# Optimization experiments

Hardware: AMD Instinct MI355X
Metric: run time of the kernel (lower is better)

Reference implementation:

```python
import jax, jax.numpy as jnp
import numpy as np

H, NH, L, S, B, V = 512, 8, 6, 2048, 2, 32000
DH = H // NH
EPS = 1e-5


def posenc(h, s):
    pos = jnp.arange(s, dtype=jnp.float32)[:, None]
    div = jnp.power(10000.0, jnp.arange(0, h, 2, dtype=jnp.float32) / h)
    pe = jnp.zeros((s, h), dtype=jnp.float32)
    pe = pe.at[:, 0::2].set(jnp.sin(pos / div))
    pe = pe.at[:, 1::2].set(jnp.cos(pos / div))
    return pe


def layernorm(x, g, b):
    mu = jnp.mean(x, axis=-1, keepdims=True)
    var = jnp.mean(jnp.square(x - mu), axis=-1, keepdims=True)
    return (x - mu) * jax.lax.rsqrt(var + EPS) * g + b


def setup_inputs() -> dict:
    key = jax.random.key(0)
    ks = jax.random.split(key, 16)
    sc = 0.02
    return {
        "src": jax.random.randint(ks[0], (B, S), 0, V),
        "mask": jnp.ones((B, 1, 1, S), dtype=jnp.int32),
        "emb": jax.random.normal(ks[1], (V, H), jnp.float32) * sc,
        "Wq": jax.random.normal(ks[2], (L, H, H), jnp.float32) * sc,
        "bq": jnp.zeros((L, H), jnp.float32),
        "Wk": jax.random.normal(ks[3], (L, H, H), jnp.float32) * sc,
        "bk": jnp.zeros((L, H), jnp.float32),
        "Wv": jax.random.normal(ks[4], (L, H, H), jnp.float32) * sc,
        "bv": jnp.zeros((L, H), jnp.float32),
        "Wo": jax.random.normal(ks[5], (L, H, H), jnp.float32) * sc,
        "bo": jnp.zeros((L, H), jnp.float32),
        "gamma": jnp.ones((L, H), jnp.float32),
        "beta": jnp.zeros((L, H), jnp.float32),
        "W1": jax.random.normal(ks[6], (L, H, 4 * H), jnp.float32) * sc,
        "b1": jnp.zeros((L, 4 * H), jnp.float32),
        "W2": jax.random.normal(ks[7], (L, 4 * H, H), jnp.float32) * sc,
        "b2": jnp.zeros((L, H), jnp.float32),
    }


def reference(src, mask, emb, Wq, bq, Wk, bk, Wv, bv, Wo, bo, gamma, beta, W1, b1, W2, b2):
    x = emb[src] + posenc(H, S)[None, :, :]  # [B,S,H]
    for i in range(L):
        q = (x @ Wq[i] + bq[i]).reshape(B, S, NH, DH).transpose(0, 2, 1, 3)
        k = (x @ Wk[i] + bk[i]).reshape(B, S, NH, DH).transpose(0, 2, 1, 3)
        v = (x @ Wv[i] + bv[i]).reshape(B, S, NH, DH).transpose(0, 2, 1, 3)
        scores = jnp.einsum("bhqd,bhkd->bhqk", q, k) / jnp.sqrt(jnp.float32(DH))
        scores = jnp.where(mask == 0, jnp.float32(-1e20), scores)
        attn = jax.nn.softmax(scores, axis=-1)
        av = jnp.einsum("bhqk,bhkd->bhqd", attn, v)
        attn_out = av.transpose(0, 2, 1, 3).reshape(B, S, H) @ Wo[i] + bo[i]
        # NOTE: same LayerNorm params applied to both sublayers (as in source)
        res = x + layernorm(attn_out, gamma[i], beta[i])
        ffn = jax.nn.relu(res @ W1[i] + b1[i]) @ W2[i] + b2[i]
        x = res + layernorm(ffn, gamma[i], beta[i])
    return x
```

## Files before the change

kernel.cpp:

```cpp
#include <hip/hip_runtime.h>
#include <math.h>

#define HDIM 512
#define NHEAD 8
#define NLAYER 6
#define SEQ 2048
#define BATCH 2
#define DHEAD 64
#define TOKENS (BATCH*SEQ)
#define FFND (4*HDIM)
#define QSTR 1536

typedef unsigned short u16;
typedef unsigned long long u64;
typedef __attribute__((ext_vector_type(8))) short short8;
typedef __attribute__((ext_vector_type(4))) float f32x4;

__device__ __forceinline__ u16 f2b(float f) {
  unsigned u = __float_as_uint(f);
  u += 0x7FFFu + ((u >> 16) & 1u);
  return (u16)(u >> 16);
}

__device__ __forceinline__ unsigned cvtpk_bf16(float lo, float hi) {
  unsigned r;
  asm("v_cvt_pk_bf16_f32 %0, %1, %2" : "=v"(r) : "v"(lo), "v"(hi));
  return r;
}

__device__ __forceinline__ void gload_lds16(const u16* g, u16* l) {
  __builtin_amdgcn_global_load_lds((const __attribute__((address_space(1))) void*)g,
                                   (__attribute__((address_space(3))) void*)l, 16, 0, 0);
}

__global__ void embed_pe(const int* __restrict__ src, const float* __restrict__ emb,
                         float* __restrict__ X, u16* __restrict__ Xb) {
  int tok = blockIdx.x;
  int lane = threadIdx.x;
  int s = tok & (SEQ - 1);
  int c0 = lane * 8;
  const float* e = emb + (long)src[tok] * HDIM + c0;
  float v[8];
#pragma unroll
  for (int j = 0; j < 8; j++) {
    int c = c0 + j;
    float arg = (float)s * exp2f(-(float)(c & ~1) * 0.02595256917f);
    v[j] = e[j] + ((c & 1) ? cosf(arg) : sinf(arg));
  }
  float* xp = X + (long)tok * HDIM + c0;
#pragma unroll
  for (int j = 0; j < 8; j++) xp[j] = v[j];
  u16 hb[8];
#pragma unroll
  for (int j = 0; j < 8; j++) hb[j] = f2b(v[j]);
  uint4 pk;
  pk.x = hb[0] | ((unsigned)hb[1] << 16);
  pk.y = hb[2] | ((unsigned)hb[3] << 16);
  pk.z = hb[4] | ((unsigned)hb[5] << 16);
  pk.w = hb[6] | ((unsigned)hb[7] << 16);
  *(uint4*)(Xb + (long)tok * HDIM + c0) = pk;
}

__global__ void maskprep(const int* __restrict__ mask, u64* __restrict__ mb) {
  int t = threadIdx.x;
  int b = t >> 5, tile = t & 31;
  const int* m = mask + b * SEQ + tile * 64;
  u64 w = 0;
#pragma unroll
  for (int j = 0; j < 64; j++) w |= (u64)(m[j] != 0) << j;
  mb[t] = w;
}

__global__ __launch_bounds__(256) void prep_weights(
    const float* __restrict__ Wq, const float* __restrict__ Wk, const float* __restrict__ Wv,
    const float* __restrict__ Wo, const float* __restrict__ W1, const float* __restrict__ W2,
    const float* __restrict__ bq, const float* __restrict__ bk, const float* __restrict__ bv,
    u16* __restrict__ Wqkvt, u16* __restrict__ Wot, u16* __restrict__ W1t, u16* __restrict__ W2t,
    float* __restrict__ bqkv) {
  int t = blockIdx.x;
  int tid = threadIdx.x;
  if (t == 768) {
    for (int i = tid; i < 1536; i += 256)
      bqkv[i] = (i < 512) ? bq[i] : (i < 1024) ? bk[i - 512] : bv[i - 1024];
    return;
  }
  const float* src; u16* dst; int K, N, kt, nt; long drow0 = 0;
  if (t < 192)      { int m = t / 64, r = t % 64; src = (m==0)?Wq:(m==1)?Wk:Wv; dst = Wqkvt; drow0 = (long)m*512; K=512;  N=512;  kt=r/8;  nt=r%8; }
  else if (t < 256) { int r = t - 192; src = Wo; dst = Wot; K=512;  N=512;  kt=r/8;  nt=r%8; }
  else if (t < 512) { int r = t - 256; src = W1; dst = W1t; K=512;  N=2048; kt=r/32; nt=r%32; }
  else              { int r = t - 512; src = W2; dst = W2t; K=2048; N=512;  kt=r/8;  nt=r%8; }
  __shared__ __align__(16) u16 Lt[64 * 72];
  int kl = tid >> 2;
#pragma unroll
  for (int rr = 0; rr < 4; rr++) {
    int cl = (tid & 3) * 4 + rr * 16;
    float4 v = *(const float4*)(src + (long)(kt * 64 + kl) * N + nt * 64 + cl);
    Lt[(cl + 0) * 72 + kl] = f2b(v.x);
    Lt[(cl + 1) * 72 + kl] = f2b(v.y);
    Lt[(cl + 2) * 72 + kl] = f2b(v.z);
    Lt[(cl + 3) * 72 + kl] = f2b(v.w);
  }
  __syncthreads();
  int nl = tid >> 2;
  int kc = (tid & 3) * 16;
  u16* dp = dst + (drow0 + nt * 64 + nl) * (long)K + kt * 64 + kc;
  *(uint4*)dp       = *(const uint4*)&Lt[nl * 72 + kc];
  *(uint4*)(dp + 8) = *(const uint4*)&Lt[nl * 72 + kc + 8];
}

__global__ __launch_bounds__(256) void vtranspose(const u16* __restrict__ QKV,
                                                  u16* __restrict__ Vtb) {
  __shared__ __align__(16) u16 Lt[64 * 72];
  int tid = threadIdx.x;
  int bh = blockIdx.y, b = bh >> 3, h = bh & 7;
  int s0 = blockIdx.x * 64;
  const u16* vsrc = QKV + (long)(b * SEQ + s0) * QSTR + 1024 + h * DHEAD;
  int key = tid >> 2, dc = (tid & 3) * 16;
  const u16* vp = vsrc + (long)key * QSTR + dc;
  uint4 v0 = *(const uint4*)vp;
  uint4 v1 = *(const uint4*)(vp + 8);
  unsigned vr[8] = { v0.x, v0.y, v0.z, v0.w, v1.x, v1.y, v1.z, v1.w };
#pragma unroll
  for (int j = 0; j < 8; j++) {
    Lt[(dc + 2 * j) * 72 + key]     = (u16)vr[j];
    Lt[(dc + 2 * j + 1) * 72 + key] = (u16)(vr[j] >> 16);
  }
  __syncthreads();
  int d = tid >> 2, kc = (tid & 3) * 16;
  u16* dst = Vtb + ((long)bh * DHEAD + d) * SEQ + s0 + kc;
  *(uint4*)dst       = *(const uint4*)&Lt[d * 72 + kc];
  *(uint4*)(dst + 8) = *(const uint4*)&Lt[d * 72 + kc + 8];
}

template <int BM, int BN, bool RELU, bool WF32, bool WB16>
__global__ __launch_bounds__(256) void gemm_tn(const u16* __restrict__ A,
                                               const u16* __restrict__ Bt,
                                               const float* __restrict__ bias,
                                               float* __restrict__ Cf,
                                               u16* __restrict__ Cb,
                                               int M, int N, int K) {
  constexpr int NF = BN / 32;
  constexpr int MF = BM / 32;
  __shared__ __align__(16) u16 As[2][BM * 32];
  __shared__ __align__(16) u16 Bs[2][BN * 32];
  int tid = threadIdx.x;
  int wave = tid >> 6, lane = tid & 63;
  int ln = lane & 15, hi = lane >> 4;
  int wm = wave >> 1, wn = wave & 1;
  int m0 = blockIdx.y * BM, n0 = blockIdx.x * BN;

  f32x4 acc[MF][NF] = {};

  int srow = lane >> 2;
  int skc  = (lane & 3) * 8;

  auto issue = [&](int kt, int buf) {
    int k0 = kt * 32;
#pragma unroll
    for (int j = 0; j < BM / 64; j++) {
      int row = (wave * (BM / 64) + j) * 16 + srow;
      gload_lds16(A + (long)(m0 + row) * K + k0 + skc, &As[buf][row * 32 + skc]);
    }
#pragma unroll
    for (int j = 0; j < BN / 64; j++) {
      int row = (wave * (BN / 64) + j) * 16 + srow;
      gload_lds16(Bt + (long)(n0 + row) * K + k0 + skc, &Bs[buf][row * 32 + skc]);
    }
  };

  int NT = K / 32;
  issue(0, 0);
  __syncthreads();
  for (int kt = 0; kt < NT; kt++) {
    int buf = kt & 1;
    if (kt + 1 < NT) issue(kt + 1, buf ^ 1);
    short8 af[MF], bf[NF];
#pragma unroll
    for (int mt = 0; mt < MF; mt++)
      af[mt] = *(const short8*)&As[buf][(wm * (BM / 2) + mt * 16 + ln) * 32 + 8 * hi];
#pragma unroll
    for (int nt = 0; nt < NF; nt++)
      bf[nt] = *(const short8*)&Bs[buf][(wn * (BN / 2) + nt * 16 + ln) * 32 + 8 * hi];
#pragma unroll
    for (int mt = 0; mt < MF; mt++)
#pragma unroll
      for (int nt = 0; nt < NF; nt++)
        acc[mt][nt] = __builtin_amdgcn_mfma_f32_16x16x32_bf16(af[mt], bf[nt], acc[mt][nt], 0, 0, 0);
    __syncthreads();
  }

#pragma unroll
  for (int mt = 0; mt < MF; mt++)
#pragma unroll
    for (int nt = 0; nt < NF; nt++)
#pragma unroll
      for (int r = 0; r < 4; r++) {
        int row = m0 + wm * (BM / 2) + mt * 16 + hi * 4 + r;
        int col = n0 + wn * (BN / 2) + nt * 16 + ln;
        float v = acc[mt][nt][r] + bias[col];
        if (RELU) v = fmaxf(v, 0.0f);
        if (WF32) Cf[(long)row * N + col] = v;
        if (WB16) Cb[(long)row * N + col] = f2b(v);
      }
}

__global__ __launch_bounds__(256) void attention(const u16* __restrict__ QKV,
                                                 const u16* __restrict__ Vtb,
                                                 const u64* __restrict__ maskb,
                                                 float* __restrict__ Opart,
                                                 float* __restrict__ Lpart) {
  __shared__ __align__(16) u16 Ks[2][64 * 64];
  __shared__ __align__(16) u16 Vs[2][64 * 64];
  __shared__ u64 Msk[SEQ / 64];
  int tid = threadIdx.x, w = tid >> 6, lane = tid & 63;
  int ln = lane & 15, hi = lane >> 4;
  int h0 = hi & 1, h1 = hi >> 1, ln7 = ln & 7;
  int lin = blockIdx.x;
  int lid = (lin & 7) * 128 + (lin >> 3);
  int bh = lid >> 6, qt = (lid >> 1) & 31, kz = lid & 1;
  int b = bh >> 3, h = bh & 7;
  int q0 = qt * 64 + w * 16;
  const u16* qbase = QKV + (long)b * SEQ * QSTR + h * DHEAD;
  const u16* kbase = qbase + 512;
  const u16* vtbase = Vtb + (long)bh * DHEAD * SEQ;

  short8 qf[2];
#pragma unroll
  for (int ks = 0; ks < 2; ks++)
    qf[ks] = *(const short8*)(qbase + (long)(q0 + ln) * QSTR + ks * 32 + 8 * hi);

  u64 mw0 = 0;
  if (tid < SEQ / 64) mw0 = maskb[b * (SEQ / 64) + tid];

  int sr0 = tid >> 3, sc = tid & 7;
  const u16 *kp0, *kp1, *vp0, *vp1;
  {
    int r1 = sr0 + 32;
    int key0 = (sr0 & 7) | ((sr0 & 0x18) << 1) | ((sr0 & 0x20) >> 2);
    int key1 = (r1 & 7) | ((r1 & 0x18) << 1) | ((r1 & 0x20) >> 2);
    kp0 = kbase + (long)key0 * QSTR + (sc ^ (sr0 & 7)) * 8;
    kp1 = kbase + (long)key1 * QSTR + (sc ^ (r1 & 7)) * 8;
    vp0 = vtbase + (long)sr0 * SEQ + (sc ^ (sr0 & 7)) * 8;
    vp1 = vtbase + (long)r1 * SEQ + (sc ^ (r1 & 7)) * 8;
  }
  int d0 = sr0 * 64 + sc * 8, d1 = d0 + 2048;

  auto issue = [&](int t, int buf) {
    long ko = (long)t * (64 * QSTR);
    int vo = t * 64;
    gload_lds16(kp0 + ko, &Ks[buf][d0]);
    gload_lds16(kp1 + ko, &Ks[buf][d1]);
    gload_lds16(vp0 + vo, &Vs[buf][d0]);
    gload_lds16(vp1 + vo, &Vs[buf][d1]);
  };

  f32x4 o[4] = {};
  float lsum = 0.0f;
  const int t0 = kz * 16;
  const int NTL = 16;

  issue(t0, 0);
  issue(t0 + 1, 1);
  if (tid < SEQ / 64) Msk[tid] = mw0;
  asm volatile("s_waitcnt vmcnt(4)" ::: "memory");
  __builtin_amdgcn_sched_barrier(0);
  __builtin_amdgcn_s_barrier();
  __builtin_amdgcn_sched_barrier(0);

  for (int ti = 0; ti < NTL; ti++) {
    int buf = ti & 1;
    u64 mw = Msk[t0 + ti];

    f32x4 s[4] = {};
    __builtin_amdgcn_s_setprio(1);
#pragma unroll
    for (int ks = 0; ks < 2; ks++)
#pragma unroll
      for (int kb = 0; kb < 4; kb++) {
        short8 kf = *(const short8*)&Ks[buf][(kb * 16 + ln) * 64 + (((ks << 2) + hi) ^ ln7) * 8];
        s[kb] = __builtin_amdgcn_mfma_f32_16x16x32_bf16(kf, qf[ks], s[kb], 0, 0, 0);
      }
    __builtin_amdgcn_s_setprio(0);

    unsigned D[4][2];
    if (mw == 0xFFFFFFFFFFFFFFFFull) {
#pragma unroll
      for (int kb = 0; kb < 4; kb++) {
        float p[4];
#pragma unroll
        for (int r = 0; r < 4; r++) {
          float pv = __expf(s[kb][r] * 0.125f);
          lsum += pv;
          p[r] = pv;
        }
        D[kb][0] = cvtpk_bf16(p[0], p[1]);
        D[kb][1] = cvtpk_bf16(p[2], p[3]);
      }
    } else {
      unsigned shb = h1 * 16 + h0 * 4;
      u64 mws = mw >> shb;
      unsigned nib[4] = { (unsigned)mws & 0xFu, (unsigned)(mws >> 32) & 0xFu,
                          (unsigned)(mws >> 8) & 0xFu, (unsigned)(mws >> 40) & 0xFu };
#pragma unroll
      for (int kb = 0; kb < 4; kb++) {
        float p[4];
#pragma unroll
        for (int r = 0; r < 4; r++) {
          float pv = __expf(s[kb][r] * 0.125f);
          pv = ((nib[kb] >> r) & 1u) ? pv : 0.0f;
          lsum += pv;
          p[r] = pv;
        }
        D[kb][0] = cvtpk_bf16(p[0], p[1]);
        D[kb][1] = cvtpk_bf16(p[2], p[3]);
      }
    }

    short8 pb[2];
#pragma unroll
    for (int ks = 0; ks < 2; ks++) {
      unsigned own0 = h0 ? D[2 + ks][0] : D[ks][0];
      unsigned own1 = h0 ? D[2 + ks][1] : D[ks][1];
      unsigned snd0 = h0 ? D[ks][0] : D[2 + ks][0];
      unsigned snd1 = h0 ? D[ks][1] : D[2 + ks][1];
      unsigned rc0 = (unsigned)__shfl_xor((int)snd0, 16);
      unsigned rc1 = (unsigned)__shfl_xor((int)snd1, 16);
      union { unsigned u[4]; short8 v; } pu;
      pu.u[0] = h0 ? rc0 : own0;
      pu.u[1] = h0 ? rc1 : own1;
      pu.u[2] = h0 ? own0 : rc0;
      pu.u[3] = h0 ? own1 : rc1;
      pb[ks] = pu.v;
    }

    __builtin_amdgcn_s_setprio(1);
#pragma unroll
    for (int ks = 0; ks < 2; ks++)
#pragma unroll
      for (int mb = 0; mb < 4; mb++) {
        short8 vf = *(const short8*)&Vs[buf][(mb * 16 + ln) * 64 + (((ks << 2) + hi) ^ ln7) * 8];
        o[mb] = __builtin_amdgcn_mfma_f32_16x16x32_bf16(vf, pb[ks], o[mb], 0, 0, 0);
      }
    __builtin_amdgcn_s_setprio(0);

    asm volatile("s_waitcnt lgkmcnt(0)" ::: "memory");
    __builtin_amdgcn_sched_barrier(0);
    __builtin_amdgcn_s_barrier();
    __builtin_amdgcn_sched_barrier(0);
    if (ti + 2 < NTL) {
      issue(t0 + ti + 2, buf);
      asm volatile("s_waitcnt vmcnt(4)" ::: "memory");
    } else {
      asm volatile("s_waitcnt vmcnt(0)" ::: "memory");
    }
    __builtin_amdgcn_sched_barrier(0);
    __builtin_amdgcn_s_barrier();
    __builtin_amdgcn_sched_barrier(0);
  }

  lsum += __shfl_xor(lsum, 16);
  lsum += __shfl_xor(lsum, 32);

  float* OpB = Opart + (long)lid * 4096 + w * 1024;
#pragma unroll
  for (int mb = 0; mb < 4; mb++)
    *(f32x4*)&OpB[ln * 64 + mb * 16 + hi * 4] = o[mb];
  if (hi == 0) Lpart[(long)lid * 64 + w * 16 + ln] = lsum;
}

__global__ __launch_bounds__(256) void attn_merge(const float* __restrict__ Op,
                                                  const float* __restrict__ Lp,
                                                  u16* __restrict__ Og) {
  int lin = blockIdx.x;
  int mlid = (lin & 7) * 64 + (lin >> 3);
  int bh = mlid >> 5, qt = mlid & 31;
  int b = bh >> 3, h = bh & 7;
  int tid = threadIdx.x;
  __shared__ float Ls[64];
  if (tid < 64) Ls[tid] = 1.0f / (Lp[(long)mlid * 128 + tid] + Lp[(long)mlid * 128 + 64 + tid]);
  __syncthreads();
  const float* P0 = Op + (long)mlid * 8192;
  const float* P1 = P0 + 4096;
  u16* obase = Og + (long)b * SEQ * HDIM + (long)qt * 64 * HDIM + h * DHEAD;
#pragma unroll
  for (int j = 0; j < 4; j++) {
    int flat = j * 1024 + tid * 4;
    int row = flat >> 6, c = flat & 63;
    float4 a = *(const float4*)&P0[flat];
    float4 bb = *(const float4*)&P1[flat];
    float rl = Ls[row];
    uint2 val;
    val.x = cvtpk_bf16((a.x + bb.x) * rl, (a.y + bb.y) * rl);
    val.y = cvtpk_bf16((a.z + bb.z) * rl, (a.w + bb.w) * rl);
    *(uint2*)(obase + (long)row * HDIM + c) = val;
  }
}

__global__ __launch_bounds__(256) void ln_residual(const float* __restrict__ Xin,
                                                   const float* __restrict__ T0,
                                                   const float* __restrict__ gamma,
                                                   const float* __restrict__ beta,
                                                   float* __restrict__ Xout,
                                                   u16* __restrict__ Xb) {
  int tid = threadIdx.x, w = tid >> 6, lane = tid & 63;
  int row = blockIdx.x * 4 + w;
  const float* t0 = T0 + (long)row * HDIM;
  int c0 = lane * 8;
  float v[8];
  {
    float4 a0 = *(const float4*)(t0 + c0);
    float4 b0 = *(const float4*)(t0 + c0 + 4);
    v[0] = a0.x; v[1] = a0.y; v[2] = a0.z; v[3] = a0.w;
    v[4] = b0.x; v[5] = b0.y; v[6] = b0.z; v[7] = b0.w;
  }
  float sum = 0.0f;
#pragma unroll
  for (int j = 0; j < 8; j++) sum += v[j];
#pragma unroll
  for (int off = 32; off; off >>= 1) sum += __shfl_xor(sum, off);
  float mu = sum * (1.0f / HDIM);
  float sq = 0.0f;
#pragma unroll
  for (int j = 0; j < 8; j++) { float d = v[j] - mu; sq += d * d; }
#pragma unroll
  for (int off = 32; off; off >>= 1) sq += __shfl_xor(sq, off);
  float rs = rsqrtf(sq * (1.0f / HDIM) + 1e-5f);
  const float* xin = Xin + (long)row * HDIM + c0;
  float* xout = Xout + (long)row * HDIM + c0;
  u16 hb[8];
#pragma unroll
  for (int j = 0; j < 8; j++) {
    int c = c0 + j;
    float y = xin[j] + (v[j] - mu) * rs * gamma[c] + beta[c];
    xout[j] = y;
    hb[j] = f2b(y);
  }
  uint4 pk;
  pk.x = hb[0] | ((unsigned)hb[1] << 16);
  pk.y = hb[2] | ((unsigned)hb[3] << 16);
  pk.z = hb[4] | ((unsigned)hb[5] << 16);
  pk.w = hb[6] | ((unsigned)hb[7] << 16);
  *(uint4*)(Xb + (long)row * HDIM + c0) = pk;
}

extern "C" void kernel_launch(void* const* d_in, const int* in_sizes, int n_in,
                              void* d_out, int out_size, void* d_ws, size_t ws_size,
                              hipStream_t stream) {
  const int*   src   = (const int*)d_in[0];
  const int*   mask  = (const int*)d_in[1];
  const float* emb   = (const float*)d_in[2];
  const float* Wq    = (const float*)d_in[3];
  const float* bq    = (const float*)d_in[4];
  const float* Wk    = (const float*)d_in[5];
  const float* bk    = (const float*)d_in[6];
  const float* Wv    = (const float*)d_in[7];
  const float* bv    = (const float*)d_in[8];
  const float* Wo    = (const float*)d_in[9];
  const float* bo    = (const float*)d_in[10];
  const float* gamma = (const float*)d_in[11];
  const float* beta  = (const float*)d_in[12];
  const float* W1    = (const float*)d_in[13];
  const float* b1    = (const float*)d_in[14];
  const float* W2    = (const float*)d_in[15];
  const float* b2    = (const float*)d_in[16];

  char* ws = (char*)d_ws;
  float* X     = (float*)(ws);
  u16*   Xb    = (u16*)(ws + (8ll << 20));
  u16*   QKVb  = (u16*)(ws + (12ll << 20));
  u16*   Mb    = (u16*)(ws + (12ll << 20));
  u16*   AVb   = (u16*)(ws + (24ll << 20));
  float* T     = (float*)(ws + (28ll << 20));
  u16*   Wqkvt = (u16*)(ws + (44ll << 20));
  u16*   Wot   = (u16*)(ws + (45ll << 20) + (512ll << 10));
  u16*   W1t   = (u16*)(ws + (46ll << 20));
  u16*   W2t   = (u16*)(ws + (48ll << 20));
  float* bqkv  = (float*)(ws + (50ll << 20));
  float* Lpart = (float*)(ws + (50ll << 20) + (512ll << 10));
  u16*   Vtb   = (u16*)(ws + (51ll << 20));
  u64*   maskbits = (u64*)(ws + (55ll << 20));
  float* Opart = T;

  embed_pe<<<dim3(TOKENS), dim3(64), 0, stream>>>(src, emb, X, Xb);
  maskprep<<<dim3(1), dim3(64), 0, stream>>>(mask, maskbits);

  for (int i = 0; i < NLAYER; i++) {
    long wo = (long)i * HDIM * HDIM;
    prep_weights<<<dim3(769), 256, 0, stream>>>(
        Wq + wo, Wk + wo, Wv + wo, Wo + wo,
        W1 + (long)i * HDIM * FFND, W2 + (long)i * FFND * HDIM,
        bq + i * HDIM, bk + i * HDIM, bv + i * HDIM,
        Wqkvt, Wot, W1t, W2t, bqkv);

    gemm_tn<128, 128, false, false, true><<<dim3(QSTR / 128, TOKENS / 128), 256, 0, stream>>>(
        Xb, Wqkvt, bqkv, nullptr, QKVb, TOKENS, QSTR, HDIM);

    vtranspose<<<dim3(SEQ / 64, BATCH * NHEAD), 256, 0, stream>>>(QKVb, Vtb);

    attention<<<dim3(1024), 256, 0, stream>>>(QKVb, Vtb, maskbits, Opart, Lpart);

    attn_merge<<<dim3(512), 256, 0, stream>>>(Opart, Lpart, AVb);

    gemm_tn<64, 64, false, true, false><<<dim3(HDIM / 64, TOKENS / 64), 256, 0, stream>>>(
        AVb, Wot, bo + i * HDIM, T, nullptr, TOKENS, HDIM, HDIM);

    ln_residual<<<dim3(TOKENS / 4), 256, 0, stream>>>(X, T, gamma + i * HDIM,
                                                      beta + i * HDIM, X, Xb);

    gemm_tn<128, 128, true, false, true><<<dim3(FFND / 128, TOKENS / 128), 256, 0, stream>>>(
        Xb, W1t, b1 + (long)i * FFND, nullptr, Mb, TOKENS, FFND, HDIM);

    gemm_tn<64, 64, false, true, false><<<dim3(HDIM / 64, TOKENS / 64), 256, 0, stream>>>(
        Mb, W2t, b2 + i * HDIM, T, nullptr, TOKENS, HDIM, FFND);

    ln_residual<<<dim3(TOKENS / 4), 256, 0, stream>>>(X, T, gamma + i * HDIM,
                                                      beta + i * HDIM, X, Xb);
  }

  hipMemcpyAsync(d_out, X, (size_t)TOKENS * HDIM * sizeof(float),
                 hipMemcpyDeviceToDevice, stream);
}
```

Measured before the change: 946.1 us.

## Double query rows per warp and split attention keys four ways

Each attention block now covers 128 query rows (32 per warp, as two 16-row groups) instead of 64, and the key sequence is split into four chunks of 8 tiles instead of two chunks of 16. Every K/V fragment loaded from LDS now feeds two MFMAs, which halves LDS traffic per FLOP and adds independent MFMA chains. The trade-off is more registers per thread and twice the partial-output traffic, since the merge kernel now sums four partials. Opart moves to its own workspace region because it has grown to twice its former size.

```diff
diff --git a/kernel.cpp b/kernel.cpp
--- a/kernel.cpp
+++ b/kernel.cpp
@@ -217,17 +217,20 @@
   int h0 = hi & 1, h1 = hi >> 1, ln7 = ln & 7;
   int lin = blockIdx.x;
   int lid = (lin & 7) * 128 + (lin >> 3);
-  int bh = lid >> 6, qt = (lid >> 1) & 31, kz = lid & 1;
+  int bh = lid >> 6, rem = lid & 63;
+  int qt = rem >> 2, kz = rem & 3;
   int b = bh >> 3, h = bh & 7;
-  int q0 = qt * 64 + w * 16;
+  int q0 = qt * 128 + w * 32;
   const u16* qbase = QKV + (long)b * SEQ * QSTR + h * DHEAD;
   const u16* kbase = qbase + 512;
   const u16* vtbase = Vtb + (long)bh * DHEAD * SEQ;
 
-  short8 qf[2];
-#pragma unroll
-  for (int ks = 0; ks < 2; ks++)
-    qf[ks] = *(const short8*)(qbase + (long)(q0 + ln) * QSTR + ks * 32 + 8 * hi);
+  short8 qf[2][2];
+#pragma unroll
+  for (int qg = 0; qg < 2; qg++)
+#pragma unroll
+    for (int ks = 0; ks < 2; ks++)
+      qf[qg][ks] = *(const short8*)(qbase + (long)(q0 + qg * 16 + ln) * QSTR + ks * 32 + 8 * hi);
 
   u64 mw0 = 0;
   if (tid < SEQ / 64) mw0 = maskb[b * (SEQ / 64) + tid];
@@ -254,10 +257,10 @@
     gload_lds16(vp1 + vo, &Vs[buf][d1]);
   };
 
-  f32x4 o[4] = {};
-  float lsum = 0.0f;
-  const int t0 = kz * 16;
-  const int NTL = 16;
+  f32x4 o[2][4] = {};
+  float lsum[2] = {0.0f, 0.0f};
+  const int t0 = kz * 8;
+  const int NTL = 8;
 
   issue(t0, 0);
   issue(t0 + 1, 1);
@@ -271,76 +274,82 @@
     int buf = ti & 1;
     u64 mw = Msk[t0 + ti];
 
-    f32x4 s[4] = {};
+    f32x4 s[2][4] = {};
     __builtin_amdgcn_s_setprio(1);
 #pragma unroll
     for (int ks = 0; ks < 2; ks++)
 #pragma unroll
       for (int kb = 0; kb < 4; kb++) {
         short8 kf = *(const short8*)&Ks[buf][(kb * 16 + ln) * 64 + (((ks << 2) + hi) ^ ln7) * 8];
-        s[kb] = __builtin_amdgcn_mfma_f32_16x16x32_bf16(kf, qf[ks], s[kb], 0, 0, 0);
+        s[0][kb] = __builtin_amdgcn_mfma_f32_16x16x32_bf16(kf, qf[0][ks], s[0][kb], 0, 0, 0);
+        s[1][kb] = __builtin_amdgcn_mfma_f32_16x16x32_bf16(kf, qf[1][ks], s[1][kb], 0, 0, 0);
       }
     __builtin_amdgcn_s_setprio(0);
 
-    unsigned D[4][2];
+    unsigned D[2][4][2];
     if (mw == 0xFFFFFFFFFFFFFFFFull) {
 #pragma unroll
-      for (int kb = 0; kb < 4; kb++) {
-        float p[4];
-#pragma unroll
-        for (int r = 0; r < 4; r++) {
-          float pv = __expf(s[kb][r] * 0.125f);
-          lsum += pv;
-          p[r] = pv;
+      for (int qg = 0; qg < 2; qg++)
+#pragma unroll
+        for (int kb = 0; kb < 4; kb++) {
+          float p[4];
+#pragma unroll
+          for (int r = 0; r < 4; r++) {
+            float pv = __expf(s[qg][kb][r] * 0.125f);
+            lsum[qg] += pv;
+            p[r] = pv;
+          }
+          D[qg][kb][0] = cvtpk_bf16(p[0], p[1]);
+          D[qg][kb][1] = cvtpk_bf16(p[2], p[3]);
         }
-        D[kb][0] = cvtpk_bf16(p[0], p[1]);
-        D[kb][1] = cvtpk_bf16(p[2], p[3]);
-      }
     } else {
       unsigned shb = h1 * 16 + h0 * 4;
       u64 mws = mw >> shb;
       unsigned nib[4] = { (unsigned)mws & 0xFu, (unsigned)(mws >> 32) & 0xFu,
                           (unsigned)(mws >> 8) & 0xFu, (unsigned)(mws >> 40) & 0xFu };
 #pragma unroll
-      for (int kb = 0; kb < 4; kb++) {
-        float p[4];
-#pragma unroll
-        for (int r = 0; r < 4; r++) {
-          float pv = __expf(s[kb][r] * 0.125f);
-          pv = ((nib[kb] >> r) & 1u) ? pv : 0.0f;
-          lsum += pv;
-          p[r] = pv;
+      for (int qg = 0; qg < 2; qg++)
+#pragma unroll
+        for (int kb = 0; kb < 4; kb++) {
+          float p[4];
+#pragma unroll
+          for (int r = 0; r < 4; r++) {
+            float pv = __expf(s[qg][kb][r] * 0.125f);
+            pv = ((nib[kb] >> r) & 1u) ? pv : 0.0f;
+            lsum[qg] += pv;
+            p[r] = pv;
+          }
+          D[qg][kb][0] = cvtpk_bf16(p[0], p[1]);
+          D[qg][kb][1] = cvtpk_bf16(p[2], p[3]);
         }
-        D[kb][0] = cvtpk_bf16(p[0], p[1]);
-        D[kb][1] = cvtpk_bf16(p[2], p[3]);
+    }
+
+    __builtin_amdgcn_s_setprio(1);
+#pragma unroll
+    for (int ks = 0; ks < 2; ks++) {
+      short8 pb[2];
+#pragma unroll
+      for (int qg = 0; qg < 2; qg++) {
+        unsigned own0 = h0 ? D[qg][2 + ks][0] : D[qg][ks][0];
+        unsigned own1 = h0 ? D[qg][2 + ks][1] : D[qg][ks][1];
+        unsigned snd0 = h0 ? D[qg][ks][0] : D[qg][2 + ks][0];
+        unsigned snd1 = h0 ? D[qg][ks][1] : D[qg][2 + ks][1];
+        unsigned rc0 = (unsigned)__shfl_xor((int)snd0, 16);
+        unsigned rc1 = (unsigned)__shfl_xor((int)snd1, 16);
+        union { unsigned u[4]; short8 v; } pu;
+        pu.u[0] = h0 ? rc0 : own0;
+        pu.u[1] = h0 ? rc1 : own1;
+        pu.u[2] = h0 ? own0 : rc0;
+        pu.u[3] = h0 ? own1 : rc1;
+        pb[qg] = pu.v;
+      }
+#pragma unroll
+      for (int mb = 0; mb < 4; mb++) {
+        short8 vf = *(const short8*)&Vs[buf][(mb * 16 + ln) * 64 + (((ks << 2) + hi) ^ ln7) * 8];
+        o[0][mb] = __builtin_amdgcn_mfma_f32_16x16x32_bf16(vf, pb[0], o[0][mb], 0, 0, 0);
+        o[1][mb] = __builtin_amdgcn_mfma_f32_16x16x32_bf16(vf, pb[1], o[1][mb], 0, 0, 0);
       }
     }
-
-    short8 pb[2];
-#pragma unroll
-    for (int ks = 0; ks < 2; ks++) {
-      unsigned own0 = h0 ? D[2 + ks][0] : D[ks][0];
-      unsigned own1 = h0 ? D[2 + ks][1] : D[ks][1];
-      unsigned snd0 = h0 ? D[ks][0] : D[2 + ks][0];
-      unsigned snd1 = h0 ? D[ks][1] : D[2 + ks][1];
-      unsigned rc0 = (unsigned)__shfl_xor((int)snd0, 16);
-      unsigned rc1 = (unsigned)__shfl_xor((int)snd1, 16);
-      union { unsigned u[4]; short8 v; } pu;
-      pu.u[0] = h0 ? rc0 : own0;
-      pu.u[1] = h0 ? rc1 : own1;
-      pu.u[2] = h0 ? own0 : rc0;
-      pu.u[3] = h0 ? own1 : rc1;
-      pb[ks] = pu.v;
-    }
-
-    __builtin_amdgcn_s_setprio(1);
-#pragma unroll
-    for (int ks = 0; ks < 2; ks++)
-#pragma unroll
-      for (int mb = 0; mb < 4; mb++) {
-        short8 vf = *(const short8*)&Vs[buf][(mb * 16 + ln) * 64 + (((ks << 2) + hi) ^ ln7) * 8];
-        o[mb] = __builtin_amdgcn_mfma_f32_16x16x32_bf16(vf, pb[ks], o[mb], 0, 0, 0);
-      }
     __builtin_amdgcn_s_setprio(0);
 
     asm volatile("s_waitcnt lgkmcnt(0)" ::: "memory");
@@ -358,40 +367,54 @@
     __builtin_amdgcn_sched_barrier(0);
   }
 
-  lsum += __shfl_xor(lsum, 16);
-  lsum += __shfl_xor(lsum, 32);
-
-  float* OpB = Opart + (long)lid * 4096 + w * 1024;
-#pragma unroll
-  for (int mb = 0; mb < 4; mb++)
-    *(f32x4*)&OpB[ln * 64 + mb * 16 + hi * 4] = o[mb];
-  if (hi == 0) Lpart[(long)lid * 64 + w * 16 + ln] = lsum;
+#pragma unroll
+  for (int qg = 0; qg < 2; qg++) {
+    lsum[qg] += __shfl_xor(lsum[qg], 16);
+    lsum[qg] += __shfl_xor(lsum[qg], 32);
+  }
+
+  float* OpB = Opart + (long)lid * 8192 + w * 2048;
+#pragma unroll
+  for (int qg = 0; qg < 2; qg++)
+#pragma unroll
+    for (int mb = 0; mb < 4; mb++)
+      *(f32x4*)&OpB[(qg * 16 + ln) * 64 + mb * 16 + hi * 4] = o[qg][mb];
+  if (hi == 0) {
+    Lpart[(long)lid * 128 + w * 32 + ln]      = lsum[0];
+    Lpart[(long)lid * 128 + w * 32 + 16 + ln] = lsum[1];
+  }
 }
 
 __global__ __launch_bounds__(256) void attn_merge(const float* __restrict__ Op,
                                                   const float* __restrict__ Lp,
                                                   u16* __restrict__ Og) {
   int lin = blockIdx.x;
-  int mlid = (lin & 7) * 64 + (lin >> 3);
-  int bh = mlid >> 5, qt = mlid & 31;
+  int mlid = (lin & 7) * 32 + (lin >> 3);
+  int bh = mlid >> 4, qt = mlid & 15;
   int b = bh >> 3, h = bh & 7;
   int tid = threadIdx.x;
-  __shared__ float Ls[64];
-  if (tid < 64) Ls[tid] = 1.0f / (Lp[(long)mlid * 128 + tid] + Lp[(long)mlid * 128 + 64 + tid]);
+  __shared__ float Ls[128];
+  long lbase = (long)mlid * 4 * 128;
+  if (tid < 128) {
+    float l = Lp[lbase + tid] + Lp[lbase + 128 + tid] +
+              Lp[lbase + 256 + tid] + Lp[lbase + 384 + tid];
+    Ls[tid] = 1.0f / l;
+  }
   __syncthreads();
-  const float* P0 = Op + (long)mlid * 8192;
-  const float* P1 = P0 + 4096;
-  u16* obase = Og + (long)b * SEQ * HDIM + (long)qt * 64 * HDIM + h * DHEAD;
-#pragma unroll
-  for (int j = 0; j < 4; j++) {
+  const float* P0 = Op + (long)mlid * 4 * 8192;
+  u16* obase = Og + (long)b * SEQ * HDIM + (long)qt * 128 * HDIM + h * DHEAD;
+#pragma unroll
+  for (int j = 0; j < 8; j++) {
     int flat = j * 1024 + tid * 4;
     int row = flat >> 6, c = flat & 63;
-    float4 a = *(const float4*)&P0[flat];
-    float4 bb = *(const float4*)&P1[flat];
+    float4 a0 = *(const float4*)&P0[flat];
+    float4 a1 = *(const float4*)&P0[8192 + flat];
+    float4 a2 = *(const float4*)&P0[16384 + flat];
+    float4 a3 = *(const float4*)&P0[24576 + flat];
     float rl = Ls[row];
     uint2 val;
-    val.x = cvtpk_bf16((a.x + bb.x) * rl, (a.y + bb.y) * rl);
-    val.y = cvtpk_bf16((a.z + bb.z) * rl, (a.w + bb.w) * rl);
+    val.x = cvtpk_bf16((a0.x + a1.x + a2.x + a3.x) * rl, (a0.y + a1.y + a2.y + a3.y) * rl);
+    val.y = cvtpk_bf16((a0.z + a1.z + a2.z + a3.z) * rl, (a0.w + a1.w + a2.w + a3.w) * rl);
     *(uint2*)(obase + (long)row * HDIM + c) = val;
   }
 }
@@ -479,7 +502,7 @@
   float* Lpart = (float*)(ws + (50ll << 20) + (512ll << 10));
   u16*   Vtb   = (u16*)(ws + (51ll << 20));
   u64*   maskbits = (u64*)(ws + (55ll << 20));
-  float* Opart = T;
+  float* Opart = (float*)(ws + (56ll << 20));
 
   embed_pe<<<dim3(TOKENS), dim3(64), 0, stream>>>(src, emb, X, Xb);
   maskprep<<<dim3(1), dim3(64), 0, stream>>>(mask, maskbits);
@@ -499,7 +522,7 @@
 
     attention<<<dim3(1024), 256, 0, stream>>>(QKVb, Vtb, maskbits, Opart, Lpart);
 
-    attn_merge<<<dim3(512), 256, 0, stream>>>(Opart, Lpart, AVb);
+    attn_merge<<<dim3(256), 256, 0, stream>>>(Opart, Lpart, AVb);
 
     gemm_tn<64, 64, false, true, false><<<dim3(HDIM / 64, TOKENS / 64), 256, 0, stream>>>(
         AVb, Wot, bo + i * HDIM, T, nullptr, TOKENS, HDIM, HDIM);
```

Result: no change. 959.6 us (+1.4%).
